# Optimization experiments

Hardware: AMD Instinct MI355X
Metric: run time of the kernel (lower is better)

## Reference

```python
import jax, jax.numpy as jnp
import numpy as np

HIDDEN = 2048
QK_DIM = 2048
NUM_HEADS = 16
HEAD_DIM = QK_DIM // NUM_HEADS  # 128; RoPE rotates this many dims per head
B, T = 4, 2048
EPS = 1e-5


def setup_inputs() -> dict:
    key = jax.random.key(0)
    ks = jax.random.split(key, 10)
    return {
        "q_state": jax.random.normal(ks[0], (B, T, HIDDEN), jnp.float32),
        "k_state": jax.random.normal(ks[1], (B, T, HIDDEN), jnp.float32),
        "v_state": jax.random.normal(ks[2], (B, T, HIDDEN), jnp.float32),
        # torch Linear weights: [out_features, in_features], no bias
        "Wq": jax.random.normal(ks[3], (QK_DIM, HIDDEN), jnp.float32) * 0.02,
        "Wk": jax.random.normal(ks[4], (QK_DIM, HIDDEN), jnp.float32) * 0.02,
        "Wv": jax.random.normal(ks[5], (HIDDEN, HIDDEN), jnp.float32) * 0.02,
        "negator": jnp.asarray(1.0, jnp.float32),
        "q_gamma": jnp.ones((2 * QK_DIM,), jnp.float32),
        "q_beta": jnp.zeros((2 * QK_DIM,), jnp.float32),
        "k_gamma": jnp.ones((2 * QK_DIM,), jnp.float32),
        "k_beta": jnp.zeros((2 * QK_DIM,), jnp.float32),
        "offset": 0,
    }


def _layer_norm(x, gamma, beta):
    mu = jnp.mean(x, axis=-1, keepdims=True)
    var = jnp.mean(jnp.square(x - mu), axis=-1, keepdims=True)
    return (x - mu) * jax.lax.rsqrt(var + EPS) * gamma + beta


def _split_heads(x, n_heads):
    b, t, d = x.shape
    return x.reshape(b, t, n_heads, d // n_heads).transpose(0, 2, 1, 3)  # b h t f


def _rotate_half(x):
    # interleaved pairs: (x1, x2) -> (-x2, x1)
    x2 = x.reshape(*x.shape[:-1], x.shape[-1] // 2, 2)
    return jnp.stack((-x2[..., 1], x2[..., 0]), axis=-1).reshape(x.shape)


def _apply_rope(x, offset, rot_dim):
    # x: [b, h, t, f]; rotate first rot_dim features, pass the rest through
    t = (jnp.arange(x.shape[-2]) + offset).astype(jnp.float32)
    inv_freq = 1.0 / (10000.0 ** (jnp.arange(0, rot_dim, 2, dtype=jnp.float32) / rot_dim))
    freqs = t[:, None] * inv_freq[None, :]           # [t, rot_dim/2]
    freqs = jnp.repeat(freqs, 2, axis=-1)            # [t, rot_dim] interleaved
    cos, sin = jnp.cos(freqs), jnp.sin(freqs)
    xl, xr = x[..., :rot_dim], x[..., rot_dim:]
    xl = xl * cos + _rotate_half(xl) * sin
    return jnp.concatenate([xl, xr], axis=-1)


def reference(q_state, k_state, v_state, Wq, Wk, Wv, negator,
              q_gamma, q_beta, k_gamma, k_beta, offset):
    q = jnp.einsum("btd,fd->btf", q_state, Wq)
    k = jnp.einsum("btd,fd->btf", k_state, Wk)
    v = jnp.einsum("btd,fd->btf", v_state, Wv)
    q = jnp.concatenate((q, negator - q), axis=-1)   # [b, t, 2*QK_DIM]
    k = jnp.concatenate((k, negator - k), axis=-1)
    q = _layer_norm(q, q_gamma, q_beta)
    k = _layer_norm(k, k_gamma, k_beta)
    q = _split_heads(q, NUM_HEADS)                   # [b, h, t, 2*HEAD_DIM]
    k = _split_heads(k, NUM_HEADS)
    v = _split_heads(v, NUM_HEADS)                   # [b, h, t, HIDDEN/h]
    q = _apply_rope(q, offset, HEAD_DIM)
    k = _apply_rope(k, offset, HEAD_DIM)
    return q, k, v
```

## Files before the change

kernel.cpp:

```cpp
#include <hip/hip_runtime.h>
#include <hip/hip_fp16.h>

#define TDIM 2048
#define BDIM 4
#define MROWS 8192
#define NDIM 2048
#define KDIM 2048
#define NH 16

typedef __attribute__((ext_vector_type(8))) _Float16 f16x8;
typedef __attribute__((ext_vector_type(4))) _Float16 f16x4;
typedef __attribute__((ext_vector_type(4))) float f32x4;

__device__ __forceinline__ void load16_to_lds(const _Float16* g, _Float16* l) {
  __builtin_amdgcn_global_load_lds((const __attribute__((address_space(1))) void*)g,
                                   (__attribute__((address_space(3))) void*)l,
                                   16, 0, 0);
}

#define WAITBAR(N) do { \
  asm volatile("s_waitcnt vmcnt(" #N ")" ::: "memory"); \
  __builtin_amdgcn_s_barrier(); \
  __builtin_amdgcn_sched_barrier(0); \
} while (0)

__global__ __launch_bounds__(256) void cvt6_kernel(
    const float* __restrict__ s0, const float* __restrict__ s1,
    const float* __restrict__ s2, const float* __restrict__ s3,
    const float* __restrict__ s4, const float* __restrict__ s5,
    _Float16* __restrict__ d0, _Float16* __restrict__ d1,
    _Float16* __restrict__ d2, _Float16* __restrict__ d3,
    _Float16* __restrict__ d4, _Float16* __restrict__ d5) {
  const int z = blockIdx.z;
  const float* s; _Float16* d; int n;
  switch (z) {
    case 0: s = s0; d = d0; n = MROWS * KDIM; break;
    case 1: s = s1; d = d1; n = MROWS * KDIM; break;
    case 2: s = s2; d = d2; n = MROWS * KDIM; break;
    case 3: s = s3; d = d3; n = NDIM * KDIM; break;
    case 4: s = s4; d = d4; n = NDIM * KDIM; break;
    default: s = s5; d = d5; n = NDIM * KDIM; break;
  }
  const int n8 = n >> 3;
  const int stride = gridDim.x * blockDim.x;
  for (int i = blockIdx.x * blockDim.x + threadIdx.x; i < n8; i += stride) {
    float4 f0 = ((const float4*)s)[i * 2 + 0];
    float4 f1 = ((const float4*)s)[i * 2 + 1];
    f16x8 h;
    h[0] = (_Float16)f0.x; h[1] = (_Float16)f0.y;
    h[2] = (_Float16)f0.z; h[3] = (_Float16)f0.w;
    h[4] = (_Float16)f1.x; h[5] = (_Float16)f1.y;
    h[6] = (_Float16)f1.z; h[7] = (_Float16)f1.w;
    ((f16x8*)d)[i] = h;
  }
}

__global__ __launch_bounds__(256) void rope_fill_kernel(
    const int* __restrict__ offset_p, float* __restrict__ tab) {
  const int idx = blockIdx.x * blockDim.x + threadIdx.x;
  if (idx >= TDIM * 64) return;
  const int t = idx >> 6, p = idx & 63;
  const float tpos = (float)(t + offset_p[0]);
  const float invf = exp2f(-(float)p * 0.20762050592854797f);
  float sv, cv;
  sincosf(tpos * invf, &sv, &cv);
  tab[idx * 2 + 0] = cv;
  tab[idx * 2 + 1] = sv;
}

__global__ __launch_bounds__(512, 2) void gemm_kernel(
    const _Float16* __restrict__ A0, const _Float16* __restrict__ A1,
    const _Float16* __restrict__ A2,
    const _Float16* __restrict__ W0, const _Float16* __restrict__ W1,
    const _Float16* __restrict__ W2,
    _Float16* __restrict__ qraw, _Float16* __restrict__ kraw,
    float* __restrict__ vout) {
  __shared__ __align__(16) _Float16 lds[4][2][8192];

  int lin = (blockIdx.z * gridDim.y + blockIdx.y) * gridDim.x + blockIdx.x;
  lin = (lin & 7) * 96 + (lin >> 3);
  const int z  = lin >> 8;
  const int ty = (lin >> 3) & 31;
  const int tx = lin & 7;

  const _Float16* __restrict__ A  = (z == 0) ? A0 : ((z == 1) ? A1 : A2);
  const _Float16* __restrict__ Wt = (z == 0) ? W0 : ((z == 1) ? W1 : W2);
  const int m0 = ty * 256;
  const int n0 = tx * 256;

  const int tid  = threadIdx.x;
  const int wave = tid >> 6;
  const int lane = tid & 63;
  const int m_in = lane & 15;
  const int kq   = lane >> 4;
  const int wave_m = wave >> 2;
  const int wave_n = wave & 3;

  f32x4 acc[8][4];
  const f32x4 z4 = {0.f, 0.f, 0.f, 0.f};
#pragma unroll
  for (int i = 0; i < 8; ++i)
#pragma unroll
    for (int j = 0; j < 4; ++j) acc[i][j] = z4;

  const int P0 = tid * 16;
  const int P1 = (512 + tid) * 16;
  const int L0 = P0 ^ (((P0 >> 7) & 3) << 4);
  const int L1 = P1 ^ (((P1 >> 7) & 3) << 4);
  const _Float16* srcA0 = A  + (size_t)(m0 + (L0 >> 6)) * KDIM + ((L0 & 63) >> 1);
  const _Float16* srcA1 = A  + (size_t)(m0 + (L1 >> 6)) * KDIM + ((L1 & 63) >> 1);
  const _Float16* srcB0 = Wt + (size_t)(n0 + (L0 >> 6)) * KDIM + ((L0 & 63) >> 1);
  const _Float16* srcB1 = Wt + (size_t)(n0 + (L1 >> 6)) * KDIM + ((L1 & 63) >> 1);
  const int dst0 = (wave * 64) * 8;
  const int dst1 = (512 + wave * 64) * 8;

  int offA[8], offB[4];
#pragma unroll
  for (int mi = 0; mi < 8; ++mi) {
    const int r = wave_m * 128 + mi * 16 + m_in;
    offA[mi] = r * 64 + ((kq ^ ((r >> 1) & 3)) << 4);
  }
#pragma unroll
  for (int ni = 0; ni < 4; ++ni) {
    const int r = wave_n * 64 + ni * 16 + m_in;
    offB[ni] = r * 64 + ((kq ^ ((r >> 1) & 3)) << 4);
  }

  auto stage = [&](int kt) {
    _Float16* base = &lds[kt & 3][0][0];
    const int ko = kt * 32;
    load16_to_lds(srcA0 + ko, base + dst0);
    load16_to_lds(srcA1 + ko, base + dst1);
    load16_to_lds(srcB0 + ko, base + 8192 + dst0);
    load16_to_lds(srcB1 + ko, base + 8192 + dst1);
  };

  auto compute = [&](int kt) {
    const char* Ab = (const char*)&lds[kt & 3][0][0];
    const char* Bb = (const char*)&lds[kt & 3][1][0];
    f16x8 a[8], b[4];
#pragma unroll
    for (int mi = 0; mi < 8; ++mi) a[mi] = *(const f16x8*)(Ab + offA[mi]);
#pragma unroll
    for (int ni = 0; ni < 4; ++ni) b[ni] = *(const f16x8*)(Bb + offB[ni]);
    __builtin_amdgcn_s_setprio(1);
#pragma unroll
    for (int mi = 0; mi < 8; ++mi)
#pragma unroll
      for (int ni = 0; ni < 4; ++ni)
        acc[mi][ni] = __builtin_amdgcn_mfma_f32_16x16x32_f16(a[mi], b[ni], acc[mi][ni], 0, 0, 0);
    __builtin_amdgcn_s_setprio(0);
  };

  stage(0); stage(1); stage(2);
  WAITBAR(8);

#pragma unroll 1
  for (int kt = 0; kt < KDIM / 32 - 3; ++kt) {
    stage(kt + 3);
    compute(kt);
    WAITBAR(8);
  }
  compute(KDIM / 32 - 3); WAITBAR(4);
  compute(KDIM / 32 - 2); WAITBAR(0);
  compute(KDIM / 32 - 1);

  const int rbase = kq * 4;
  const int wm = wave_m * 128;
  const int wn = wave_n * 64;
  if (z < 2) {
    _Float16* __restrict__ raw = (z == 0) ? qraw : kraw;
#pragma unroll
    for (int mi = 0; mi < 8; ++mi) {
      const int m = m0 + wm + mi * 16 + rbase;
#pragma unroll
      for (int ni = 0; ni < 4; ++ni) {
        const int n = n0 + wn + ni * 16 + m_in;
#pragma unroll
        for (int r = 0; r < 4; ++r)
          raw[(size_t)(m + r) * NDIM + n] = (_Float16)acc[mi][ni][r];
      }
    }
  } else {
#pragma unroll
    for (int mi = 0; mi < 8; ++mi) {
      const int mb = m0 + wm + mi * 16 + rbase;
#pragma unroll
      for (int ni = 0; ni < 4; ++ni) {
        const int n = n0 + wn + ni * 16 + m_in;
        const int h = n >> 7, dd = n & 127;
#pragma unroll
        for (int r = 0; r < 4; ++r) {
          const int m = mb + r;
          const int b = m >> 11, t = m & 2047;
          vout[(((size_t)(b * NH + h) * TDIM) + t) * 128 + dd] = acc[mi][ni][r];
        }
      }
    }
  }
}

__global__ __launch_bounds__(256) void ln_rope_kernel(
    const _Float16* __restrict__ qraw, const _Float16* __restrict__ kraw,
    const float* __restrict__ negator,
    const float* __restrict__ q_gamma, const float* __restrict__ q_beta,
    const float* __restrict__ k_gamma, const float* __restrict__ k_beta,
    const float* __restrict__ rope_tab,
    float* __restrict__ out) {
  const int row = blockIdx.x;
  const int mat = blockIdx.y;
  const _Float16* __restrict__ raw = mat ? kraw : qraw;
  const float* __restrict__ gamma = mat ? k_gamma : q_gamma;
  const float* __restrict__ beta  = mat ? k_beta  : q_beta;
  float* __restrict__ outb = out + (size_t)mat * ((size_t)BDIM * NH * TDIM * 256);

  const float c = negator[0];
  const float mu = 0.5f * c;
  const int tid = threadIdx.x;

  __shared__ __align__(16) float vals[2048];
  __shared__ float wred[4];

  const int b = row >> 11, t = row & 2047;

  f16x8 hv = ((const f16x8*)(raw + (size_t)row * 2048))[tid];
  float v[8];
  float ss = 0.f;
#pragma unroll
  for (int j = 0; j < 8; ++j) {
    float x = (float)hv[j] - mu;
    v[j] = x;
    ss += x * x;
  }
  ((float4*)vals)[tid * 2 + 0] = make_float4(v[0], v[1], v[2], v[3]);
  ((float4*)vals)[tid * 2 + 1] = make_float4(v[4], v[5], v[6], v[7]);

#pragma unroll
  for (int o = 32; o > 0; o >>= 1) ss += __shfl_down(ss, o, 64);
  if ((tid & 63) == 0) wred[tid >> 6] = ss;
  __syncthreads();
  const float var = (wred[0] + wred[1] + wred[2] + wred[3]) * (1.0f / 2048.0f);
  const float rstd = rsqrtf(var + 1e-5f);

  const float4* __restrict__ tab4 = (const float4*)(rope_tab + (size_t)t * 128);

#pragma unroll
  for (int j = 0; j < 4; ++j) {
    const int g0 = j * 1024 + tid * 4;
    const float sgn = (g0 < 2048) ? 1.f : -1.f;
    const float4 val = ((const float4*)vals)[(g0 & 2047) >> 2];
    const float4 gm  = ((const float4*)gamma)[g0 >> 2];
    const float4 bt  = ((const float4*)beta)[g0 >> 2];
    float y0 = sgn * val.x * rstd * gm.x + bt.x;
    float y1 = sgn * val.y * rstd * gm.y + bt.y;
    float y2 = sgn * val.z * rstd * gm.z + bt.z;
    float y3 = sgn * val.w * rstd * gm.w + bt.w;

    const int h  = g0 >> 8;
    const int d0 = g0 & 255;
    float4 res;
    if (d0 < 128) {
      const float4 cs = tab4[d0 >> 2];
      res.x = y0 * cs.x - y1 * cs.y;
      res.y = y1 * cs.x + y0 * cs.y;
      res.z = y2 * cs.z - y3 * cs.w;
      res.w = y3 * cs.z + y2 * cs.w;
    } else {
      res = make_float4(y0, y1, y2, y3);
    }
    ((float4*)(outb + (((size_t)(b * NH + h) * TDIM) + t) * 256))[d0 >> 2] = res;
  }
}

extern "C" void kernel_launch(void* const* d_in, const int* in_sizes, int n_in,
                              void* d_out, int out_size, void* d_ws, size_t ws_size,
                              hipStream_t stream) {
  (void)in_sizes; (void)n_in; (void)out_size; (void)ws_size;
  const float* q_state = (const float*)d_in[0];
  const float* k_state = (const float*)d_in[1];
  const float* v_state = (const float*)d_in[2];
  const float* Wq = (const float*)d_in[3];
  const float* Wk = (const float*)d_in[4];
  const float* Wv = (const float*)d_in[5];
  const float* negator = (const float*)d_in[6];
  const float* q_gamma = (const float*)d_in[7];
  const float* q_beta  = (const float*)d_in[8];
  const float* k_gamma = (const float*)d_in[9];
  const float* k_beta  = (const float*)d_in[10];
  const int* offset    = (const int*)d_in[11];

  float* out = (float*)d_out;
  float* vout = out + (size_t)2 * BDIM * NH * TDIM * 256;

  _Float16* Aq   = (_Float16*)d_ws;
  _Float16* Ak   = Aq + (size_t)MROWS * KDIM;
  _Float16* Av   = Ak + (size_t)MROWS * KDIM;
  _Float16* Wq16 = Av + (size_t)MROWS * KDIM;
  _Float16* Wk16 = Wq16 + (size_t)NDIM * KDIM;
  _Float16* Wv16 = Wk16 + (size_t)NDIM * KDIM;
  _Float16* qraw = Wv16 + (size_t)NDIM * KDIM;
  _Float16* kraw = qraw + (size_t)MROWS * NDIM;

  float* rope_tab = (float*)Wq16;

  cvt6_kernel<<<dim3(2048, 1, 6), dim3(256), 0, stream>>>(
      q_state, k_state, v_state, Wq, Wk, Wv, Aq, Ak, Av, Wq16, Wk16, Wv16);

  gemm_kernel<<<dim3(8, 32, 3), dim3(512), 0, stream>>>(
      Aq, Ak, Av, Wq16, Wk16, Wv16, qraw, kraw, vout);

  rope_fill_kernel<<<dim3(512), dim3(256), 0, stream>>>(offset, rope_tab);

  ln_rope_kernel<<<dim3(8192, 2), dim3(256), 0, stream>>>(
      qraw, kraw, negator, q_gamma, q_beta, k_gamma, k_beta, rope_tab, out);
}
```

Measured before the change: 744.8 us.

## Split GEMM k-step into two phases, stage epilogue via LDS, fold rope fill into converter

Each GEMM k-step is split into two halves. Every half reads its own LDS fragments, issues half of the next async global-to-LDS load, waits on lgkmcnt and then runs half of the MFMAs, so load issue is interleaved with compute. The q/k fp16 epilogue now goes through LDS so each thread writes coalesced 16-byte global stores instead of scattered 2-byte ones. The RoPE table fill moves into the conversion kernel as an extra grid slice, which removes one launch, and the table now gets its own workspace region. The change adds an extra barrier per k-step and two syncthreads in the epilogue.

```diff
diff --git a/kernel.cpp b/kernel.cpp
--- a/kernel.cpp
+++ b/kernel.cpp
@@ -24,14 +24,33 @@
   __builtin_amdgcn_sched_barrier(0); \
 } while (0)
 
-__global__ __launch_bounds__(256) void cvt6_kernel(
+#define LGKM0_FENCE() do { \
+  asm volatile("s_waitcnt lgkmcnt(0)" ::: "memory"); \
+  __builtin_amdgcn_sched_barrier(0); \
+} while (0)
+
+__global__ __launch_bounds__(256) void cvt7_kernel(
     const float* __restrict__ s0, const float* __restrict__ s1,
     const float* __restrict__ s2, const float* __restrict__ s3,
     const float* __restrict__ s4, const float* __restrict__ s5,
     _Float16* __restrict__ d0, _Float16* __restrict__ d1,
     _Float16* __restrict__ d2, _Float16* __restrict__ d3,
-    _Float16* __restrict__ d4, _Float16* __restrict__ d5) {
+    _Float16* __restrict__ d4, _Float16* __restrict__ d5,
+    const int* __restrict__ offset_p, float* __restrict__ rope_tab) {
   const int z = blockIdx.z;
+  if (z == 6) {
+    const int idx = blockIdx.x * blockDim.x + threadIdx.x;
+    if (idx < TDIM * 64) {
+      const int t = idx >> 6, p = idx & 63;
+      const float tpos = (float)(t + offset_p[0]);
+      const float invf = exp2f(-(float)p * 0.20762050592854797f);
+      float sv, cv;
+      sincosf(tpos * invf, &sv, &cv);
+      rope_tab[idx * 2 + 0] = cv;
+      rope_tab[idx * 2 + 1] = sv;
+    }
+    return;
+  }
   const float* s; _Float16* d; int n;
   switch (z) {
     case 0: s = s0; d = d0; n = MROWS * KDIM; break;
@@ -55,19 +74,6 @@
   }
 }
 
-__global__ __launch_bounds__(256) void rope_fill_kernel(
-    const int* __restrict__ offset_p, float* __restrict__ tab) {
-  const int idx = blockIdx.x * blockDim.x + threadIdx.x;
-  if (idx >= TDIM * 64) return;
-  const int t = idx >> 6, p = idx & 63;
-  const float tpos = (float)(t + offset_p[0]);
-  const float invf = exp2f(-(float)p * 0.20762050592854797f);
-  float sv, cv;
-  sincosf(tpos * invf, &sv, &cv);
-  tab[idx * 2 + 0] = cv;
-  tab[idx * 2 + 1] = sv;
-}
-
 __global__ __launch_bounds__(512, 2) void gemm_kernel(
     const _Float16* __restrict__ A0, const _Float16* __restrict__ A1,
     const _Float16* __restrict__ A2,
@@ -126,60 +132,93 @@
     offB[ni] = r * 64 + ((kq ^ ((r >> 1) & 3)) << 4);
   }
 
-  auto stage = [&](int kt) {
+  auto stageA = [&](int kt) {
     _Float16* base = &lds[kt & 3][0][0];
     const int ko = kt * 32;
     load16_to_lds(srcA0 + ko, base + dst0);
     load16_to_lds(srcA1 + ko, base + dst1);
+  };
+  auto stageB = [&](int kt) {
+    _Float16* base = &lds[kt & 3][0][0];
+    const int ko = kt * 32;
     load16_to_lds(srcB0 + ko, base + 8192 + dst0);
     load16_to_lds(srcB1 + ko, base + 8192 + dst1);
   };
 
-  auto compute = [&](int kt) {
+  f16x8 a[8], b[4];
+
+  auto kstep_p1 = [&](int kt, int stage_kt) {
     const char* Ab = (const char*)&lds[kt & 3][0][0];
     const char* Bb = (const char*)&lds[kt & 3][1][0];
-    f16x8 a[8], b[4];
 #pragma unroll
     for (int mi = 0; mi < 8; ++mi) a[mi] = *(const f16x8*)(Ab + offA[mi]);
-#pragma unroll
-    for (int ni = 0; ni < 4; ++ni) b[ni] = *(const f16x8*)(Bb + offB[ni]);
+    b[0] = *(const f16x8*)(Bb + offB[0]);
+    b[1] = *(const f16x8*)(Bb + offB[1]);
+    if (stage_kt >= 0) stageA(stage_kt);
+    LGKM0_FENCE();
     __builtin_amdgcn_s_setprio(1);
 #pragma unroll
     for (int mi = 0; mi < 8; ++mi)
 #pragma unroll
-      for (int ni = 0; ni < 4; ++ni)
+      for (int ni = 0; ni < 2; ++ni)
+        acc[mi][ni] = __builtin_amdgcn_mfma_f32_16x16x32_f16(a[mi], b[ni], acc[mi][ni], 0, 0, 0);
+    __builtin_amdgcn_s_setprio(0);
+    __builtin_amdgcn_s_barrier();
+    __builtin_amdgcn_sched_barrier(0);
+  };
+  auto kstep_p2 = [&](int kt, int stage_kt) {
+    const char* Bb = (const char*)&lds[kt & 3][1][0];
+    b[2] = *(const f16x8*)(Bb + offB[2]);
+    b[3] = *(const f16x8*)(Bb + offB[3]);
+    if (stage_kt >= 0) stageB(stage_kt);
+    LGKM0_FENCE();
+    __builtin_amdgcn_s_setprio(1);
+#pragma unroll
+    for (int mi = 0; mi < 8; ++mi)
+#pragma unroll
+      for (int ni = 2; ni < 4; ++ni)
         acc[mi][ni] = __builtin_amdgcn_mfma_f32_16x16x32_f16(a[mi], b[ni], acc[mi][ni], 0, 0, 0);
     __builtin_amdgcn_s_setprio(0);
   };
 
-  stage(0); stage(1); stage(2);
+  stageA(0); stageB(0); stageA(1); stageB(1); stageA(2); stageB(2);
   WAITBAR(8);
 
 #pragma unroll 1
   for (int kt = 0; kt < KDIM / 32 - 3; ++kt) {
-    stage(kt + 3);
-    compute(kt);
+    kstep_p1(kt, kt + 3);
+    kstep_p2(kt, kt + 3);
     WAITBAR(8);
   }
-  compute(KDIM / 32 - 3); WAITBAR(4);
-  compute(KDIM / 32 - 2); WAITBAR(0);
-  compute(KDIM / 32 - 1);
+  kstep_p1(KDIM / 32 - 3, -1); kstep_p2(KDIM / 32 - 3, -1); WAITBAR(4);
+  kstep_p1(KDIM / 32 - 2, -1); kstep_p2(KDIM / 32 - 2, -1); WAITBAR(0);
+  kstep_p1(KDIM / 32 - 1, -1); kstep_p2(KDIM / 32 - 1, -1);
 
   const int rbase = kq * 4;
   const int wm = wave_m * 128;
   const int wn = wave_n * 64;
   if (z < 2) {
     _Float16* __restrict__ raw = (z == 0) ? qraw : kraw;
+    _Float16* cst = &lds[0][0][0];
+    __syncthreads();
 #pragma unroll
     for (int mi = 0; mi < 8; ++mi) {
-      const int m = m0 + wm + mi * 16 + rbase;
+      const int row = wm + mi * 16 + rbase;
 #pragma unroll
       for (int ni = 0; ni < 4; ++ni) {
-        const int n = n0 + wn + ni * 16 + m_in;
+        const int col = wn + ni * 16 + m_in;
 #pragma unroll
         for (int r = 0; r < 4; ++r)
-          raw[(size_t)(m + r) * NDIM + n] = (_Float16)acc[mi][ni][r];
+          cst[(row + r) * 256 + col] = (_Float16)acc[mi][ni][r];
       }
+    }
+    __syncthreads();
+#pragma unroll
+    for (int j = 0; j < 16; ++j) {
+      const int c = j * 512 + tid;
+      const int row = c >> 5, col8 = (c & 31) * 8;
+      *(f16x8*)&raw[(size_t)(m0 + row) * NDIM + n0 + col8] =
+          *(const f16x8*)&cst[row * 256 + col8];
     }
   } else {
 #pragma unroll
@@ -300,17 +339,15 @@
   _Float16* Wv16 = Wk16 + (size_t)NDIM * KDIM;
   _Float16* qraw = Wv16 + (size_t)NDIM * KDIM;
   _Float16* kraw = qraw + (size_t)MROWS * NDIM;
-
-  float* rope_tab = (float*)Wq16;
-
-  cvt6_kernel<<<dim3(2048, 1, 6), dim3(256), 0, stream>>>(
-      q_state, k_state, v_state, Wq, Wk, Wv, Aq, Ak, Av, Wq16, Wk16, Wv16);
+  float* rope_tab = (float*)(kraw + (size_t)MROWS * NDIM);
+
+  cvt7_kernel<<<dim3(2048, 1, 7), dim3(256), 0, stream>>>(
+      q_state, k_state, v_state, Wq, Wk, Wv, Aq, Ak, Av, Wq16, Wk16, Wv16,
+      offset, rope_tab);
 
   gemm_kernel<<<dim3(8, 32, 3), dim3(512), 0, stream>>>(
       Aq, Ak, Av, Wq16, Wk16, Wv16, qraw, kraw, vout);
 
-  rope_fill_kernel<<<dim3(512), dim3(256), 0, stream>>>(offset, rope_tab);
-
   ln_rope_kernel<<<dim3(8192, 2), dim3(256), 0, stream>>>(
       qraw, kraw, negator, q_gamma, q_beta, k_gamma, k_beta, rope_tab, out);
 }
```

After: 735.4 us. Within noise of the previous version (-1.3%).
